# Performance work log

Hardware: AMD Instinct MI355X
Metric: run time of the kernel (lower is better)

The kernel has to match this reference:

```python
import jax, jax.numpy as jnp
import numpy as np

BS, L, D = 128, 256, 512
H, DK = 2, 256  # heads, head dim
EPS_BN = 1e-5


def _lin(x, W, b):
    # torch Linear: W is (out, in)
    return jnp.einsum('...i,oi->...o', x, W) + b


def _bn(x, g, b, m, v):
    # eval-mode BatchNorm over channel axis = last axis of x
    return (x - m) * (g * jax.lax.rsqrt(v + EPS_BN)) + b


def setup_inputs() -> dict:
    key = jax.random.key(0)
    ks = iter(jax.random.split(key, 64))
    rn = lambda shape, s=0.02: jax.random.normal(next(ks), shape, dtype=jnp.float32) * s
    inp = {}
    inp['cap_emb'] = jax.random.normal(next(ks), (BS, L, D), dtype=jnp.float32)
    inp['lengths'] = jax.random.randint(next(ks), (BS,), 1, L + 1, dtype=jnp.int64 if jax.config.jax_enable_x64 else jnp.int32)
    # GA linears q,k,v
    for nm in ('Wq', 'Wk', 'Wv'):
        inp[nm] = rn((D, D))
    for nm in ('bq', 'bk', 'bv'):
        inp[nm] = rn((D,))
    inp['Wfq'] = rn((DK, DK)); inp['bfq'] = rn((DK,))
    inp['Wfk'] = rn((DK, DK)); inp['bfk'] = rn((DK,))
    inp['Wfg'] = rn((2 * DK, DK)); inp['bfg'] = rn((2 * DK,))
    # BatchNorm params (eval running stats)
    for pre in ('bn1', 'bn2', 'bn3'):
        inp[pre + '_g'] = 1.0 + rn((D,), 0.1)
        inp[pre + '_b'] = rn((D,), 0.1)
        inp[pre + '_m'] = rn((D,), 0.1)
        inp[pre + '_v'] = jax.random.uniform(next(ks), (D,), minval=0.5, maxval=1.5, dtype=jnp.float32)
    # Conv1d weights, torch layout (out, in, k)
    inp['Wc2'] = rn((D, D, 2)); inp['bc2'] = rn((D,))
    inp['Wc3'] = rn((D, D, 3)); inp['bc3'] = rn((D,))
    # MLP 512 -> 1024 -> 512
    inp['Wm1'] = rn((2 * D, D)); inp['bm1'] = rn((2 * D,))
    inp['Wm2'] = rn((D, 2 * D)); inp['bm2'] = rn((D,))
    return inp


def _forward(cap_emb, Wq, bq, Wk, bk, Wv, bv, Wfq, bfq, Wfk, bfk, Wfg, bfg,
             bn1_g, bn1_b, bn1_m, bn1_v, Wc2, bc2, bn2_g, bn2_b, bn2_m, bn2_v,
             Wc3, bc3, bn3_g, bn3_b, bn3_m, bn3_v, Wm1, bm1, Wm2, bm2, lengths):
    bs, seq, dim = cap_emb.shape
    # ---- GA: gated self-attention ----
    def split_heads(x):
        return x.reshape(bs, seq, H, DK).transpose(0, 2, 1, 3)  # [bs,h,seq,dk]
    q = split_heads(_lin(cap_emb, Wq, bq))
    k = split_heads(_lin(cap_emb, Wk, bk))
    v = split_heads(_lin(cap_emb, Wv, bv))
    G = _lin(q, Wfq, bfq) * _lin(k, Wfk, bfk)
    M = jax.nn.sigmoid(_lin(G, Wfg, bfg))  # [bs,h,seq,2*dk]
    qg = q * M[..., :DK]
    kg = k * M[..., DK:]
    # torch.div(..., rounding_mode='floor') == elementwise floor of scaled scores
    scores = jnp.floor(jnp.einsum('bhqd,bhkd->bhqk', qg, kg) / jnp.sqrt(jnp.float32(DK)))
    p_attn = jax.nn.softmax(scores, axis=-1)
    x = jnp.einsum('bhqk,bhkd->bhqd', p_attn, v)
    x = x.transpose(0, 2, 1, 3).reshape(bs, seq, dim)
    # BN over features (eval), dropout is identity in eval mode
    ga_emb = cap_emb + _bn(x, bn1_g, bn1_b, bn1_m, bn1_v)
    # ---- dual conv1d branches ----
    xc = cap_emb.transpose(0, 2, 1)  # [bs, D, L]
    dn = ('NCW', 'OIW', 'NCW')
    c2 = jax.lax.conv_general_dilated(xc, Wc2, window_strides=(2,), padding='VALID', dimension_numbers=dn) + bc2[None, :, None]
    c3 = jax.lax.conv_general_dilated(xc, Wc3, window_strides=(3,), padding='VALID', dimension_numbers=dn) + bc3[None, :, None]
    f2 = jax.nn.relu(_bn(c2.transpose(0, 2, 1), bn2_g, bn2_b, bn2_m, bn2_v))
    f3 = jax.nn.relu(_bn(c3.transpose(0, 2, 1), bn3_g, bn3_b, bn3_m, bn3_v))
    ga_jw = jnp.concatenate([ga_emb, f2, f3], axis=1)
    # ---- residual MLP (dropout identity in eval) ----
    hid = jax.nn.relu(_lin(ga_jw, Wm1, bm1))
    tex_emb = _lin(hid, Wm2, bm2) + ga_jw
    # ---- length-indexed gather ----
    idx = lengths.astype(jnp.int32) - 1
    out = tex_emb[jnp.arange(bs), idx]  # [bs, D]
    # l2norm
    norm = jnp.sqrt(jnp.sum(out * out, axis=-1, keepdims=True)) + 1e-8
    return out / norm


def reference(cap_emb, lengths, Wq, bq, Wk, bk, Wv, bv, Wfq, bfq, Wfk, bfk, Wfg, bfg,
              bn1_g, bn1_b, bn1_m, bn1_v, Wc2, bc2, bn2_g, bn2_b, bn2_m, bn2_v,
              Wc3, bc3, bn3_g, bn3_b, bn3_m, bn3_v, Wm1, bm1, Wm2, bm2):
    return _forward(cap_emb, Wq, bq, Wk, bk, Wv, bv, Wfq, bfq, Wfk, bfk, Wfg, bfg,
                    bn1_g, bn1_b, bn1_m, bn1_v, Wc2, bc2, bn2_g, bn2_b, bn2_m, bn2_v,
                    Wc3, bc3, bn3_g, bn3_b, bn3_m, bn3_v, Wm1, bm1, Wm2, bm2, lengths)
```

## Files before the change

### kernel.cpp

```cpp
#include <hip/hip_runtime.h>
#include <math.h>


typedef short bf16x8 __attribute__((ext_vector_type(8)));
typedef float f32x4 __attribute__((ext_vector_type(4)));
typedef short short4v __attribute__((ext_vector_type(4)));

__device__ __forceinline__ short f2bf(float x) {
    union { float f; unsigned u; } c; c.f = x;
    unsigned r = c.u + 0x7FFFu + ((c.u >> 16) & 1u);
    return (short)(r >> 16);
}
__device__ __forceinline__ float bf2f(short h) {
    union { float f; unsigned u; } c; c.u = ((unsigned)(unsigned short)h) << 16;
    return c.f;
}
__device__ __forceinline__ void glds16(const void* g, void* l) {
    __builtin_amdgcn_global_load_lds(
        (const __attribute__((address_space(1))) void*)g,
        (__attribute__((address_space(3))) void*)l, 16, 0, 0);
}

struct CastArgs {
    const float* src[3];
    short* dst[3];
    int n4[3];
};
__global__ __launch_bounds__(256) void cast_multi(CastArgs a)
{
    const int j = blockIdx.y;
    const float4* s = (const float4*)a.src[j];
    short* d = a.dst[j];
    const int n4 = a.n4[j];
    for (int i = blockIdx.x * 256 + threadIdx.x; i < n4; i += gridDim.x * 256) {
        float4 x = s[i];
        short4v h;
        h.x = f2bf(x.x); h.y = f2bf(x.y); h.z = f2bf(x.z); h.w = f2bf(x.w);
        *(short4v*)&d[i * 4] = h;
    }
}

__global__ __launch_bounds__(256)
void compose2(const float* __restrict__ Wq, const float* __restrict__ bq,
              const float* __restrict__ Wfq, const float* __restrict__ bfq,
              const float* __restrict__ Wk, const float* __restrict__ bk,
              const float* __restrict__ Wfk, const float* __restrict__ bfk,
              short* __restrict__ WaB, float* __restrict__ ba,
              short* __restrict__ WbB, float* __restrict__ bb)
{
    __shared__ float fq[256];
    __shared__ float redc[256];
    const int op = blockIdx.x;
    const int h = op >> 8, o = op & 255;
    const int t = threadIdx.x;
    const bool second = (blockIdx.y == 1);
    const float* W  = second ? Wk  : Wq;
    const float* bv = second ? bk  : bq;
    const float* F  = second ? Wfk : Wfq;
    const float* bf = second ? bfk : bfq;
    short* WB   = second ? WbB : WaB;
    float* bout = second ? bb  : ba;

    fq[t] = F[o * 256 + t];
    redc[t] = fq[t] * bv[h * 256 + t];
    __syncthreads();
    for (int s = 128; s > 0; s >>= 1) {
        if (t < s) redc[t] += redc[t + s];
        __syncthreads();
    }
    if (t == 0) bout[op] = redc[0] + bf[o];
    float s0 = 0.f, s1 = 0.f;
    for (int d = 0; d < 256; ++d) {
        const float f = fq[d];
        const float* wr = W + (size_t)(h * 256 + d) * 512;
        s0 += f * wr[t];
        s1 += f * wr[t + 256];
    }
    const size_t ro = (size_t)op * 512;
    WB[ro + t] = f2bf(s0);
    WB[ro + 256 + t] = f2bf(s1);
}

__device__ __forceinline__ void kloop_w(
    const short* __restrict__ A, int lda,
    const short* __restrict__ B, int ldb,
    int K, int bm, short (*lds)[12288], int tid, f32x4 acc[4][4])
{
    const int lane = tid & 63;
    const int wv = tid >> 6;
    const int wr = wv >> 2, wc = wv & 3;
    const int fr = lane & 15, kc = lane >> 4;
    const int r0 = tid >> 2;
    const int e0 = (((tid & 3) ^ ((r0 >> 1) & 3))) * 8;
    const int kce = (kc ^ ((fr >> 1) & 3)) * 8;

    auto stage = [&](int ph, int k0) {
        short* b = lds[ph];
        glds16(A + (size_t)(bm + r0) * lda + k0 + e0,    b + r0 * 32 + (tid & 3) * 8);
        glds16(B + (size_t)r0 * ldb + k0 + e0,           b + 4096 + r0 * 32 + (tid & 3) * 8);
        glds16(B + (size_t)(r0 + 128) * ldb + k0 + e0,   b + 4096 + (r0 + 128) * 32 + (tid & 3) * 8);
    };

    stage(0, 0);
    __syncthreads();
    const int NS = K / 32;
    for (int s = 0; s < NS; ++s) {
        if (s + 1 < NS) stage((s + 1) & 1, (s + 1) * 32);
        const short* b = lds[s & 1];
        bf16x8 ah[4], bh[4];
#pragma unroll
        for (int i = 0; i < 4; ++i)
            ah[i] = *(const bf16x8*)&b[(wr * 64 + i * 16 + fr) * 32 + kce];
#pragma unroll
        for (int i = 0; i < 4; ++i)
            bh[i] = *(const bf16x8*)&b[4096 + (wc * 64 + i * 16 + fr) * 32 + kce];
#pragma unroll
        for (int mi = 0; mi < 4; ++mi)
#pragma unroll
            for (int ni = 0; ni < 4; ++ni)
                acc[mi][ni] = __builtin_amdgcn_mfma_f32_16x16x32_bf16(ah[mi], bh[ni], acc[mi][ni], 0, 0, 0);
        __syncthreads();
    }
}

__global__ __launch_bounds__(512)
void gemm_g(const short* __restrict__ capB,
            const short* __restrict__ WaB, const short* __restrict__ WbB,
            const float* __restrict__ ba, const float* __restrict__ bb,
            short* __restrict__ Gbuf)
{
    __shared__ short lds[2][20480];
    const int tid = threadIdx.x;
    const int bm = blockIdx.x * 128;
    const int z = blockIdx.y;
    const short* B1 = WaB + (size_t)z * 256 * 512;
    const short* B2 = WbB + (size_t)z * 256 * 512;

    const int lane = tid & 63;
    const int wv = tid >> 6;
    const int wr = wv >> 2, wc = wv & 3;
    const int fr = lane & 15, kc = lane >> 4;
    const int r0 = tid >> 2;
    const int e0 = (((tid & 3) ^ ((r0 >> 1) & 3))) * 8;
    const int kce = (kc ^ ((fr >> 1) & 3)) * 8;

    auto stage = [&](int ph, int k0) {
        short* b = lds[ph];
        glds16(capB + (size_t)(bm + r0) * 512 + k0 + e0, b + r0 * 32 + (tid & 3) * 8);
        glds16(B1 + (size_t)r0 * 512 + k0 + e0,          b + 4096 + r0 * 32 + (tid & 3) * 8);
        glds16(B1 + (size_t)(r0 + 128) * 512 + k0 + e0,  b + 4096 + (r0 + 128) * 32 + (tid & 3) * 8);
        glds16(B2 + (size_t)r0 * 512 + k0 + e0,          b + 12288 + r0 * 32 + (tid & 3) * 8);
        glds16(B2 + (size_t)(r0 + 128) * 512 + k0 + e0,  b + 12288 + (r0 + 128) * 32 + (tid & 3) * 8);
    };

    f32x4 acc1[4][4], acc2[4][4];
#pragma unroll
    for (int i = 0; i < 4; ++i)
#pragma unroll
        for (int j = 0; j < 4; ++j) {
            acc1[i][j] = (f32x4){0.f, 0.f, 0.f, 0.f};
            acc2[i][j] = (f32x4){0.f, 0.f, 0.f, 0.f};
        }

    stage(0, 0);
    __syncthreads();
    for (int s = 0; s < 16; ++s) {
        if (s + 1 < 16) stage((s + 1) & 1, (s + 1) * 32);
        const short* b = lds[s & 1];
        bf16x8 ah[4], bh[4];
#pragma unroll
        for (int i = 0; i < 4; ++i)
            ah[i] = *(const bf16x8*)&b[(wr * 64 + i * 16 + fr) * 32 + kce];
#pragma unroll
        for (int i = 0; i < 4; ++i)
            bh[i] = *(const bf16x8*)&b[4096 + (wc * 64 + i * 16 + fr) * 32 + kce];
#pragma unroll
        for (int mi = 0; mi < 4; ++mi)
#pragma unroll
            for (int ni = 0; ni < 4; ++ni)
                acc1[mi][ni] = __builtin_amdgcn_mfma_f32_16x16x32_bf16(ah[mi], bh[ni], acc1[mi][ni], 0, 0, 0);
#pragma unroll
        for (int i = 0; i < 4; ++i)
            bh[i] = *(const bf16x8*)&b[12288 + (wc * 64 + i * 16 + fr) * 32 + kce];
#pragma unroll
        for (int mi = 0; mi < 4; ++mi)
#pragma unroll
            for (int ni = 0; ni < 4; ++ni)
                acc2[mi][ni] = __builtin_amdgcn_mfma_f32_16x16x32_bf16(ah[mi], bh[ni], acc2[mi][ni], 0, 0, 0);
        __syncthreads();
    }

#pragma unroll
    for (int mi = 0; mi < 4; ++mi) {
#pragma unroll
        for (int ni = 0; ni < 4; ++ni) {
#pragma unroll
            for (int r = 0; r < 4; ++r) {
                const int row = bm + wr * 64 + mi * 16 + kc * 4 + r;
                const int col = wc * 64 + ni * 16 + fr;
                const float av  = acc1[mi][ni][r] + ba[z * 256 + col];
                const float lin = acc2[mi][ni][r] + bb[z * 256 + col];
                Gbuf[(size_t)row * 512 + z * 256 + col] = f2bf(lin * av);
            }
        }
    }
}

__global__ __launch_bounds__(512)
void gemm_kg(const short* __restrict__ Gbuf,
             const short* __restrict__ Wfg2B, const float* __restrict__ bias,
             const short* __restrict__ capB,
             const short* __restrict__ WkB, const float* __restrict__ bk,
             const float* __restrict__ qg, float* __restrict__ scorep)
{
    __shared__ short lds[2][12288];
    __shared__ float sp[128][4];
    const int tid = threadIdx.x;
    const int bm = blockIdx.x * 128;
    const int z = blockIdx.y;

    f32x4 acc1[4][4], acc2[4][4];
#pragma unroll
    for (int i = 0; i < 4; ++i)
#pragma unroll
        for (int j = 0; j < 4; ++j) {
            acc1[i][j] = (f32x4){0.f, 0.f, 0.f, 0.f};
            acc2[i][j] = (f32x4){0.f, 0.f, 0.f, 0.f};
        }

    kloop_w(Gbuf + (size_t)z * 256, 512, Wfg2B, 256, 256, bm, lds, tid, acc1);
    kloop_w(capB, 512, WkB + (size_t)z * 256 * 512, 512, 512, bm, lds, tid, acc2);

    const int lane = tid & 63;
    const int wv = tid >> 6;
    const int wr = wv >> 2, wc = wv & 3;
    const int fr = lane & 15, kc = lane >> 4;

    float qgv[4];
    float pt[4][4];
    {
        const int b = bm >> 8;
#pragma unroll
        for (int ni = 0; ni < 4; ++ni)
            qgv[ni] = qg[b * 512 + z * 256 + wc * 64 + ni * 16 + fr];
#pragma unroll
        for (int mi = 0; mi < 4; ++mi)
#pragma unroll
            for (int r = 0; r < 4; ++r) pt[mi][r] = 0.f;
    }

#pragma unroll
    for (int mi = 0; mi < 4; ++mi) {
#pragma unroll
        for (int ni = 0; ni < 4; ++ni) {
#pragma unroll
            for (int r = 0; r < 4; ++r) {
                const int col = wc * 64 + ni * 16 + fr;
                const float v = acc1[mi][ni][r] + bias[col];
                const float e = acc2[mi][ni][r] + bk[z * 256 + col];
                const float kgv = e / (1.f + expf(-v));
                pt[mi][r] += kgv * qgv[ni];
            }
        }
    }

#pragma unroll
    for (int mi = 0; mi < 4; ++mi) {
#pragma unroll
        for (int r = 0; r < 4; ++r) {
            float p = pt[mi][r];
            p += __shfl_xor(p, 1);
            p += __shfl_xor(p, 2);
            p += __shfl_xor(p, 4);
            p += __shfl_xor(p, 8);
            if (fr == 0) {
                const int row_local = wr * 64 + mi * 16 + kc * 4 + r;
                sp[row_local][wc] = p;
            }
        }
    }
    __syncthreads();
    if (tid < 128) {
        const float s = sp[tid][0] + sp[tid][1] + sp[tid][2] + sp[tid][3];
        const int row = bm + tid;
        const int b = row >> 8, j = row & 255;
        scorep[(size_t)b * 512 + z * 256 + j] = s;
    }
}

__global__ __launch_bounds__(256)
void qg_kernel(const float* __restrict__ cap,
               const short* __restrict__ Gbuf,
               const float* __restrict__ Wq, const float* __restrict__ bq,
               const float* __restrict__ Wfg, const float* __restrict__ bfg,
               const int* __restrict__ lengths, float* __restrict__ qg)
{
    __shared__ float cr[512];
    __shared__ float gs[256];
    const int b = blockIdx.x >> 1, h = blockIdx.x & 1;
    const int t = threadIdx.x;
    int r = lengths[b] - 1;
    if (r < 0) r = 0;
    if (r > 255) r = 255;
    const size_t base = ((size_t)b * 256 + r) * 512;
    cr[t] = cap[base + t];
    cr[t + 256] = cap[base + 256 + t];
    gs[t] = bf2f(Gbuf[base + h * 256 + t]);
    __syncthreads();
    const float4* wq4 = (const float4*)(Wq + (size_t)(h * 256 + t) * 512);
    float q = 0.f;
    for (int k4 = 0; k4 < 128; ++k4) {
        float4 w = wq4[k4];
        q += w.x * cr[k4 * 4 + 0] + w.y * cr[k4 * 4 + 1]
           + w.z * cr[k4 * 4 + 2] + w.w * cr[k4 * 4 + 3];
    }
    q += bq[h * 256 + t];
    const float4* w4 = (const float4*)(Wfg + (size_t)t * 256);
    float a = 0.f;
    for (int k4 = 0; k4 < 64; ++k4) {
        float4 w = w4[k4];
        a += w.x * gs[k4 * 4 + 0] + w.y * gs[k4 * 4 + 1]
           + w.z * gs[k4 * 4 + 2] + w.w * gs[k4 * 4 + 3];
    }
    a += bfg[t];
    qg[b * 512 + h * 256 + t] = q / (1.f + expf(-a));
}

__global__ __launch_bounds__(256)
void pbar_kernel(const float* __restrict__ scorep, const short* __restrict__ capB,
                 float* __restrict__ pbar)
{
    __shared__ float sc[512], red[512];
    const int b = blockIdx.y, cg = blockIdx.x;
    const int t = threadIdx.x;
#pragma unroll
    for (int i = 0; i < 2; ++i) {
        const int o = t + i * 256;
        sc[o] = floorf(scorep[(size_t)b * 512 + o] * 0.0625f);
    }
    __syncthreads();
    red[t] = sc[t]; red[t + 256] = sc[t + 256];
    __syncthreads();
    for (int s = 128; s > 0; s >>= 1) {
        if (t < s) {
            red[t] = fmaxf(red[t], red[t + s]);
            red[256 + t] = fmaxf(red[256 + t], red[256 + t + s]);
        }
        __syncthreads();
    }
    const float mx0 = red[0], mx1 = red[256];
    __syncthreads();
    const float e0 = expf(sc[t] - mx0);
    const float e1 = expf(sc[t + 256] - mx1);
    red[t] = e0; red[t + 256] = e1;
    __syncthreads();
    for (int s = 128; s > 0; s >>= 1) {
        if (t < s) { red[t] += red[t + s]; red[256 + t] += red[256 + t + s]; }
        __syncthreads();
    }
    sc[t] = e0 / red[0];
    sc[t + 256] = e1 / red[256];
    __syncthreads();

    const int c = cg * 64 + (t & 63);
    const int jg = t >> 6;
    float a0 = 0.f, a1 = 0.f;
    for (int j = jg * 64; j < jg * 64 + 64; ++j) {
        const float cv = bf2f(capB[((size_t)(b * 256 + j)) * 512 + c]);
        a0 += sc[j] * cv;
        a1 += sc[256 + j] * cv;
    }
    red[t] = a0;
    __syncthreads();
    if (t < 64) {
        const float s0 = red[t] + red[t + 64] + red[t + 128] + red[t + 192];
        pbar[b * 1024 + cg * 64 + t] = s0;
    }
    __syncthreads();
    red[t] = a1;
    __syncthreads();
    if (t < 64) {
        const float s1 = red[t] + red[t + 64] + red[t + 128] + red[t + 192];
        pbar[b * 1024 + 512 + cg * 64 + t] = s1;
    }
}

__global__ __launch_bounds__(256)
void bnx_kernel(const float* __restrict__ pbar, const float* __restrict__ cap,
                const int* __restrict__ lengths,
                const float* __restrict__ Wv, const float* __restrict__ bv,
                const float* __restrict__ g1, const float* __restrict__ b1,
                const float* __restrict__ m1, const float* __restrict__ v1,
                float* __restrict__ xga)
{
    __shared__ float pb[1024];
    const int b = blockIdx.x;
    const int t = threadIdx.x;
    int r = lengths[b] - 1;
    if (r < 0) r = 0;
    if (r > 255) r = 255;
    const size_t base = ((size_t)b * 256 + r) * 512;
    pb[t] = pbar[b * 1024 + t];
    pb[t + 256] = pbar[b * 1024 + 256 + t];
    pb[t + 512] = pbar[b * 1024 + 512 + t];
    pb[t + 768] = pbar[b * 1024 + 768 + t];
    __syncthreads();
    float x0 = 0.f, x1 = 0.f;
    {
        const float4* w4 = (const float4*)(Wv + (size_t)t * 512);
        for (int k4 = 0; k4 < 128; ++k4) {
            float4 w = w4[k4];
            x0 += w.x * pb[k4 * 4 + 0] + w.y * pb[k4 * 4 + 1]
                + w.z * pb[k4 * 4 + 2] + w.w * pb[k4 * 4 + 3];
        }
        x0 += bv[t];
    }
    {
        const float4* w4 = (const float4*)(Wv + (size_t)(t + 256) * 512);
        for (int k4 = 0; k4 < 128; ++k4) {
            float4 w = w4[k4];
            x1 += w.x * pb[512 + k4 * 4 + 0] + w.y * pb[512 + k4 * 4 + 1]
                + w.z * pb[512 + k4 * 4 + 2] + w.w * pb[512 + k4 * 4 + 3];
        }
        x1 += bv[t + 256];
    }
    const int c0 = t, c1 = t + 256;
    const float s0 = g1[c0] / sqrtf(v1[c0] + 1e-5f);
    const float s1 = g1[c1] / sqrtf(v1[c1] + 1e-5f);
    xga[b * 512 + c0] = cap[base + c0] + (x0 - m1[c0]) * s0 + b1[c0];
    xga[b * 512 + c1] = cap[base + c1] + (x1 - m1[c1]) * s1 + b1[c1];
}

__global__ __launch_bounds__(256)
void mlp1(const float* __restrict__ xga, const float* __restrict__ W,
          const float* __restrict__ bias, float* __restrict__ hid)
{
    __shared__ float xs[16 * 512];
    const int r0 = blockIdx.y * 16;
    const int c0 = blockIdx.x * 64;
    for (int i = threadIdx.x; i < 2048; i += 256)
        ((float4*)xs)[i] = ((const float4*)(xga + (size_t)r0 * 512))[i];
    __syncthreads();
    const int col = c0 + (threadIdx.x & 63);
    const int rg = (threadIdx.x >> 6) * 4;
    float acc[4] = {0.f, 0.f, 0.f, 0.f};
    const float4* w4 = (const float4*)(W + (size_t)col * 512);
    for (int k4 = 0; k4 < 128; ++k4) {
        float4 w = w4[k4];
#pragma unroll
        for (int rr = 0; rr < 4; ++rr) {
            float4 x = *(const float4*)&xs[(rg + rr) * 512 + k4 * 4];
            acc[rr] += w.x * x.x + w.y * x.y + w.z * x.z + w.w * x.w;
        }
    }
    const float bb = bias[col];
#pragma unroll
    for (int rr = 0; rr < 4; ++rr)
        hid[(size_t)(r0 + rg + rr) * 1024 + col] = fmaxf(acc[rr] + bb, 0.f);
}

__global__ __launch_bounds__(256)
void mlp2(const float* __restrict__ hid, const float* __restrict__ W,
          const float* __restrict__ bias, const float* __restrict__ xga,
          float* __restrict__ tex)
{
    __shared__ float xs[16 * 1024];
    const int r0 = blockIdx.y * 16;
    const int c0 = blockIdx.x * 64;
    for (int i = threadIdx.x; i < 4096; i += 256)
        ((float4*)xs)[i] = ((const float4*)(hid + (size_t)r0 * 1024))[i];
    __syncthreads();
    const int col = c0 + (threadIdx.x & 63);
    const int rg = (threadIdx.x >> 6) * 4;
    float acc[4] = {0.f, 0.f, 0.f, 0.f};
    const float4* w4 = (const float4*)(W + (size_t)col * 1024);
    for (int k4 = 0; k4 < 256; ++k4) {
        float4 w = w4[k4];
#pragma unroll
        for (int rr = 0; rr < 4; ++rr) {
            float4 x = *(const float4*)&xs[(rg + rr) * 1024 + k4 * 4];
            acc[rr] += w.x * x.x + w.y * x.y + w.z * x.z + w.w * x.w;
        }
    }
    const float bb = bias[col];
#pragma unroll
    for (int rr = 0; rr < 4; ++rr) {
        const int row = r0 + rg + rr;
        tex[(size_t)row * 512 + col] = acc[rr] + bb + xga[(size_t)row * 512 + col];
    }
}

__global__ __launch_bounds__(256)
void norm_out(const float* __restrict__ tex, float* __restrict__ out)
{
    __shared__ float red[256];
    const int b = blockIdx.x;
    const int t = threadIdx.x;
    const float a = tex[b * 512 + t];
    const float c = tex[b * 512 + 256 + t];
    red[t] = a * a + c * c;
    __syncthreads();
    for (int s = 128; s > 0; s >>= 1) {
        if (t < s) red[t] += red[t + s];
        __syncthreads();
    }
    const float inv = 1.f / (sqrtf(red[0]) + 1e-8f);
    out[b * 512 + t] = a * inv;
    out[b * 512 + 256 + t] = c * inv;
}

extern "C" void kernel_launch(void* const* d_in, const int* in_sizes, int n_in,
                              void* d_out, int out_size, void* d_ws, size_t ws_size,
                              hipStream_t stream)
{
    const float* cap = (const float*)d_in[0];
    const int* lengths = (const int*)d_in[1];
    const float* Wq  = (const float*)d_in[2];
    const float* Wk  = (const float*)d_in[3];
    const float* Wv  = (const float*)d_in[4];
    const float* bq  = (const float*)d_in[5];
    const float* bk  = (const float*)d_in[6];
    const float* bv  = (const float*)d_in[7];
    const float* Wfq = (const float*)d_in[8];
    const float* bfq = (const float*)d_in[9];
    const float* Wfk = (const float*)d_in[10];
    const float* bfk = (const float*)d_in[11];
    const float* Wfg = (const float*)d_in[12];
    const float* bfg = (const float*)d_in[13];
    const float* g1  = (const float*)d_in[14];
    const float* b1  = (const float*)d_in[15];
    const float* m1  = (const float*)d_in[16];
    const float* v1  = (const float*)d_in[17];
    const float* Wm1 = (const float*)d_in[30];
    const float* bm1 = (const float*)d_in[31];
    const float* Wm2 = (const float*)d_in[32];
    const float* bm2 = (const float*)d_in[33];
    float* out = (float*)d_out;

    char* w = (char*)d_ws;
    const size_t MB = 1024 * 1024;
    short* capB = (short*)(w);
    short* Gbuf = (short*)(w + 32 * MB);
    char* wp = w + 64 * MB;
    short* WkB   = (short*)wp; wp += 524288;
    short* WaB   = (short*)wp; wp += 524288;
    short* WbB   = (short*)wp; wp += 524288;
    short* Wfg2B = (short*)wp; wp += 131072;
    float* ba     = (float*)wp; wp += 2048;
    float* bb     = (float*)wp; wp += 2048;
    float* qg     = (float*)wp; wp += 262144;
    float* scorep = (float*)wp; wp += 262144;
    float* pbar   = (float*)wp; wp += 524288;
    float* xga    = (float*)wp; wp += 262144;
    float* hid    = (float*)wp; wp += 524288;
    float* tex    = (float*)wp; wp += 262144;

    CastArgs ca;
    ca.src[0] = cap;          ca.dst[0] = capB;  ca.n4[0] = 4194304;
    ca.src[1] = Wk;           ca.dst[1] = WkB;   ca.n4[1] = 65536;
    ca.src[2] = Wfg + 65536;  ca.dst[2] = Wfg2B; ca.n4[2] = 16384;
    cast_multi<<<dim3(4096, 3), 256, 0, stream>>>(ca);

    compose2<<<dim3(512, 2), 256, 0, stream>>>(Wq, bq, Wfq, bfq, Wk, bk, Wfk, bfk,
                                               WaB, ba, WbB, bb);

    gemm_g<<<dim3(256, 2), 512, 0, stream>>>(capB, WaB, WbB, ba, bb, Gbuf);

    qg_kernel<<<dim3(256), 256, 0, stream>>>(cap, Gbuf, Wq, bq, Wfg, bfg, lengths, qg);

    gemm_kg<<<dim3(256, 2), 512, 0, stream>>>(Gbuf, Wfg2B, bfg + 256,
                                              capB, WkB, bk, qg, scorep);

    pbar_kernel<<<dim3(8, 128), 256, 0, stream>>>(scorep, capB, pbar);
    bnx_kernel<<<dim3(128), 256, 0, stream>>>(pbar, cap, lengths, Wv, bv, g1, b1, m1, v1, xga);

    mlp1<<<dim3(16, 8), 256, 0, stream>>>(xga, Wm1, bm1, hid);
    mlp2<<<dim3(8, 8), 256, 0, stream>>>(hid, Wm2, bm2, xga, tex);
    norm_out<<<dim3(128), 256, 0, stream>>>(tex, out);
}
```

Before: 271.2 us.

## Fuse gate GEMM with key-gate GEMM, keeping G tile in LDS

```diff
diff --git a/kernel.cpp b/kernel.cpp
--- a/kernel.cpp
+++ b/kernel.cpp
@@ -81,11 +81,18 @@
     WB[ro + 256 + t] = f2bf(s1);
 }
 
-__device__ __forceinline__ void kloop_w(
-    const short* __restrict__ A, int lda,
-    const short* __restrict__ B, int ldb,
-    int K, int bm, short (*lds)[12288], int tid, f32x4 acc[4][4])
-{
+__global__ __launch_bounds__(512)
+void gemm_gkg(const short* __restrict__ capB,
+              const short* __restrict__ WaB, const short* __restrict__ WbB,
+              const float* __restrict__ ba, const float* __restrict__ bb,
+              const short* __restrict__ Wfg2B, const float* __restrict__ bfg2,
+              const short* __restrict__ WkB, const float* __restrict__ bk,
+              const float* __restrict__ qg, float* __restrict__ scorep)
+{
+    __shared__ short smem[40960];
+    const int tid = threadIdx.x;
+    const int bm = blockIdx.x * 128;
+    const int z = blockIdx.y;
     const int lane = tid & 63;
     const int wv = tid >> 6;
     const int wr = wv >> 2, wc = wv & 3;
@@ -94,64 +101,8 @@
     const int e0 = (((tid & 3) ^ ((r0 >> 1) & 3))) * 8;
     const int kce = (kc ^ ((fr >> 1) & 3)) * 8;
 
-    auto stage = [&](int ph, int k0) {
-        short* b = lds[ph];
-        glds16(A + (size_t)(bm + r0) * lda + k0 + e0,    b + r0 * 32 + (tid & 3) * 8);
-        glds16(B + (size_t)r0 * ldb + k0 + e0,           b + 4096 + r0 * 32 + (tid & 3) * 8);
-        glds16(B + (size_t)(r0 + 128) * ldb + k0 + e0,   b + 4096 + (r0 + 128) * 32 + (tid & 3) * 8);
-    };
-
-    stage(0, 0);
-    __syncthreads();
-    const int NS = K / 32;
-    for (int s = 0; s < NS; ++s) {
-        if (s + 1 < NS) stage((s + 1) & 1, (s + 1) * 32);
-        const short* b = lds[s & 1];
-        bf16x8 ah[4], bh[4];
-#pragma unroll
-        for (int i = 0; i < 4; ++i)
-            ah[i] = *(const bf16x8*)&b[(wr * 64 + i * 16 + fr) * 32 + kce];
-#pragma unroll
-        for (int i = 0; i < 4; ++i)
-            bh[i] = *(const bf16x8*)&b[4096 + (wc * 64 + i * 16 + fr) * 32 + kce];
-#pragma unroll
-        for (int mi = 0; mi < 4; ++mi)
-#pragma unroll
-            for (int ni = 0; ni < 4; ++ni)
-                acc[mi][ni] = __builtin_amdgcn_mfma_f32_16x16x32_bf16(ah[mi], bh[ni], acc[mi][ni], 0, 0, 0);
-        __syncthreads();
-    }
-}
-
-__global__ __launch_bounds__(512)
-void gemm_g(const short* __restrict__ capB,
-            const short* __restrict__ WaB, const short* __restrict__ WbB,
-            const float* __restrict__ ba, const float* __restrict__ bb,
-            short* __restrict__ Gbuf)
-{
-    __shared__ short lds[2][20480];
-    const int tid = threadIdx.x;
-    const int bm = blockIdx.x * 128;
-    const int z = blockIdx.y;
     const short* B1 = WaB + (size_t)z * 256 * 512;
     const short* B2 = WbB + (size_t)z * 256 * 512;
-
-    const int lane = tid & 63;
-    const int wv = tid >> 6;
-    const int wr = wv >> 2, wc = wv & 3;
-    const int fr = lane & 15, kc = lane >> 4;
-    const int r0 = tid >> 2;
-    const int e0 = (((tid & 3) ^ ((r0 >> 1) & 3))) * 8;
-    const int kce = (kc ^ ((fr >> 1) & 3)) * 8;
-
-    auto stage = [&](int ph, int k0) {
-        short* b = lds[ph];
-        glds16(capB + (size_t)(bm + r0) * 512 + k0 + e0, b + r0 * 32 + (tid & 3) * 8);
-        glds16(B1 + (size_t)r0 * 512 + k0 + e0,          b + 4096 + r0 * 32 + (tid & 3) * 8);
-        glds16(B1 + (size_t)(r0 + 128) * 512 + k0 + e0,  b + 4096 + (r0 + 128) * 32 + (tid & 3) * 8);
-        glds16(B2 + (size_t)r0 * 512 + k0 + e0,          b + 12288 + r0 * 32 + (tid & 3) * 8);
-        glds16(B2 + (size_t)(r0 + 128) * 512 + k0 + e0,  b + 12288 + (r0 + 128) * 32 + (tid & 3) * 8);
-    };
 
     f32x4 acc1[4][4], acc2[4][4];
 #pragma unroll
@@ -162,11 +113,20 @@
             acc2[i][j] = (f32x4){0.f, 0.f, 0.f, 0.f};
         }
 
-    stage(0, 0);
+    auto stageA = [&](int ph, int k0) {
+        short* s = smem + ph * 20480;
+        glds16(capB + (size_t)(bm + r0) * 512 + k0 + e0, s + tid * 8);
+        glds16(B1 + (size_t)r0 * 512 + k0 + e0,          s + 4096 + tid * 8);
+        glds16(B1 + (size_t)(r0 + 128) * 512 + k0 + e0,  s + 4096 + (tid + 512) * 8);
+        glds16(B2 + (size_t)r0 * 512 + k0 + e0,          s + 12288 + tid * 8);
+        glds16(B2 + (size_t)(r0 + 128) * 512 + k0 + e0,  s + 12288 + (tid + 512) * 8);
+    };
+
+    stageA(0, 0);
     __syncthreads();
     for (int s = 0; s < 16; ++s) {
-        if (s + 1 < 16) stage((s + 1) & 1, (s + 1) * 32);
-        const short* b = lds[s & 1];
+        if (s + 1 < 16) stageA((s + 1) & 1, (s + 1) * 32);
+        const short* b = smem + (s & 1) * 20480;
         bf16x8 ah[4], bh[4];
 #pragma unroll
         for (int i = 0; i < 4; ++i)
@@ -196,58 +156,87 @@
         for (int ni = 0; ni < 4; ++ni) {
 #pragma unroll
             for (int r = 0; r < 4; ++r) {
-                const int row = bm + wr * 64 + mi * 16 + kc * 4 + r;
+                const int row = wr * 64 + mi * 16 + kc * 4 + r;
                 const int col = wc * 64 + ni * 16 + fr;
-                const float av  = acc1[mi][ni][r] + ba[z * 256 + col];
-                const float lin = acc2[mi][ni][r] + bb[z * 256 + col];
-                Gbuf[(size_t)row * 512 + z * 256 + col] = f2bf(lin * av);
+                const float g = (acc2[mi][ni][r] + bb[z * 256 + col])
+                              * (acc1[mi][ni][r] + ba[z * 256 + col]);
+                const int grp = (col >> 3) ^ ((row >> 1) & 3);
+                smem[row * 256 + grp * 8 + (col & 7)] = f2bf(g);
             }
         }
     }
-}
-
-__global__ __launch_bounds__(512)
-void gemm_kg(const short* __restrict__ Gbuf,
-             const short* __restrict__ Wfg2B, const float* __restrict__ bias,
-             const short* __restrict__ capB,
-             const short* __restrict__ WkB, const float* __restrict__ bk,
-             const float* __restrict__ qg, float* __restrict__ scorep)
-{
-    __shared__ short lds[2][12288];
-    __shared__ float sp[128][4];
-    const int tid = threadIdx.x;
-    const int bm = blockIdx.x * 128;
-    const int z = blockIdx.y;
-
-    f32x4 acc1[4][4], acc2[4][4];
+    __syncthreads();
+
+    f32x4 acc3[4][4];
 #pragma unroll
     for (int i = 0; i < 4; ++i)
 #pragma unroll
-        for (int j = 0; j < 4; ++j) {
-            acc1[i][j] = (f32x4){0.f, 0.f, 0.f, 0.f};
-            acc2[i][j] = (f32x4){0.f, 0.f, 0.f, 0.f};
-        }
-
-    kloop_w(Gbuf + (size_t)z * 256, 512, Wfg2B, 256, 256, bm, lds, tid, acc1);
-    kloop_w(capB, 512, WkB + (size_t)z * 256 * 512, 512, 512, bm, lds, tid, acc2);
-
-    const int lane = tid & 63;
-    const int wv = tid >> 6;
-    const int wr = wv >> 2, wc = wv & 3;
-    const int fr = lane & 15, kc = lane >> 4;
+        for (int j = 0; j < 4; ++j) acc3[i][j] = (f32x4){0.f, 0.f, 0.f, 0.f};
+
+    short* sB = smem + 32768;
+    for (int kk = 0; kk < 8; ++kk) {
+        const int k0 = kk * 32;
+        glds16(Wfg2B + (size_t)r0 * 256 + k0 + e0,         sB + tid * 8);
+        glds16(Wfg2B + (size_t)(r0 + 128) * 256 + k0 + e0, sB + (tid + 512) * 8);
+        __syncthreads();
+        bf16x8 ah[4], bh[4];
+#pragma unroll
+        for (int i = 0; i < 4; ++i)
+            ah[i] = *(const bf16x8*)&smem[(wr * 64 + i * 16 + fr) * 256 + k0 + kce];
+#pragma unroll
+        for (int i = 0; i < 4; ++i)
+            bh[i] = *(const bf16x8*)&sB[(wc * 64 + i * 16 + fr) * 32 + kce];
+#pragma unroll
+        for (int mi = 0; mi < 4; ++mi)
+#pragma unroll
+            for (int ni = 0; ni < 4; ++ni)
+                acc3[mi][ni] = __builtin_amdgcn_mfma_f32_16x16x32_bf16(ah[mi], bh[ni], acc3[mi][ni], 0, 0, 0);
+        __syncthreads();
+    }
+
+    const short* BK = WkB + (size_t)z * 256 * 512;
+#pragma unroll
+    for (int i = 0; i < 4; ++i)
+#pragma unroll
+        for (int j = 0; j < 4; ++j) acc2[i][j] = (f32x4){0.f, 0.f, 0.f, 0.f};
+
+    auto stageC = [&](int ph, int k0) {
+        short* s = smem + ph * 12288;
+        glds16(capB + (size_t)(bm + r0) * 512 + k0 + e0, s + tid * 8);
+        glds16(BK + (size_t)r0 * 512 + k0 + e0,          s + 4096 + tid * 8);
+        glds16(BK + (size_t)(r0 + 128) * 512 + k0 + e0,  s + 4096 + (tid + 512) * 8);
+    };
+
+    stageC(0, 0);
+    __syncthreads();
+    for (int s = 0; s < 16; ++s) {
+        if (s + 1 < 16) stageC((s + 1) & 1, (s + 1) * 32);
+        const short* b = smem + (s & 1) * 12288;
+        bf16x8 ah[4], bh[4];
+#pragma unroll
+        for (int i = 0; i < 4; ++i)
+            ah[i] = *(const bf16x8*)&b[(wr * 64 + i * 16 + fr) * 32 + kce];
+#pragma unroll
+        for (int i = 0; i < 4; ++i)
+            bh[i] = *(const bf16x8*)&b[4096 + (wc * 64 + i * 16 + fr) * 32 + kce];
+#pragma unroll
+        for (int mi = 0; mi < 4; ++mi)
+#pragma unroll
+            for (int ni = 0; ni < 4; ++ni)
+                acc2[mi][ni] = __builtin_amdgcn_mfma_f32_16x16x32_bf16(ah[mi], bh[ni], acc2[mi][ni], 0, 0, 0);
+        __syncthreads();
+    }
 
     float qgv[4];
     float pt[4][4];
-    {
-        const int b = bm >> 8;
-#pragma unroll
-        for (int ni = 0; ni < 4; ++ni)
-            qgv[ni] = qg[b * 512 + z * 256 + wc * 64 + ni * 16 + fr];
-#pragma unroll
-        for (int mi = 0; mi < 4; ++mi)
-#pragma unroll
-            for (int r = 0; r < 4; ++r) pt[mi][r] = 0.f;
-    }
+    const int b_ = bm >> 8;
+#pragma unroll
+    for (int ni = 0; ni < 4; ++ni)
+        qgv[ni] = qg[b_ * 512 + z * 256 + wc * 64 + ni * 16 + fr];
+#pragma unroll
+    for (int mi = 0; mi < 4; ++mi)
+#pragma unroll
+        for (int r = 0; r < 4; ++r) pt[mi][r] = 0.f;
 
 #pragma unroll
     for (int mi = 0; mi < 4; ++mi) {
@@ -256,7 +245,7 @@
 #pragma unroll
             for (int r = 0; r < 4; ++r) {
                 const int col = wc * 64 + ni * 16 + fr;
-                const float v = acc1[mi][ni][r] + bias[col];
+                const float v = acc3[mi][ni][r] + bfg2[col];
                 const float e = acc2[mi][ni][r] + bk[z * 256 + col];
                 const float kgv = e / (1.f + expf(-v));
                 pt[mi][r] += kgv * qgv[ni];
@@ -264,6 +253,7 @@
         }
     }
 
+    float (*sp)[4] = (float(*)[4])smem;
 #pragma unroll
     for (int mi = 0; mi < 4; ++mi) {
 #pragma unroll
@@ -290,7 +280,8 @@
 
 __global__ __launch_bounds__(256)
 void qg_kernel(const float* __restrict__ cap,
-               const short* __restrict__ Gbuf,
+               const short* __restrict__ WaB, const short* __restrict__ WbB,
+               const float* __restrict__ ba, const float* __restrict__ bb,
                const float* __restrict__ Wq, const float* __restrict__ bq,
                const float* __restrict__ Wfg, const float* __restrict__ bfg,
                const int* __restrict__ lengths, float* __restrict__ qg)
@@ -305,7 +296,23 @@
     const size_t base = ((size_t)b * 256 + r) * 512;
     cr[t] = cap[base + t];
     cr[t + 256] = cap[base + 256 + t];
-    gs[t] = bf2f(Gbuf[base + h * 256 + t]);
+    __syncthreads();
+    {
+        const bf16x8* wa8 = (const bf16x8*)(WaB + (size_t)(h * 256 + t) * 512);
+        const bf16x8* wb8 = (const bf16x8*)(WbB + (size_t)(h * 256 + t) * 512);
+        float sa = 0.f, sb = 0.f;
+        for (int k8 = 0; k8 < 64; ++k8) {
+            bf16x8 wa = wa8[k8];
+            bf16x8 wb = wb8[k8];
+#pragma unroll
+            for (int j = 0; j < 8; ++j) {
+                const float c = cr[k8 * 8 + j];
+                sa += bf2f(wa[j]) * c;
+                sb += bf2f(wb[j]) * c;
+            }
+        }
+        gs[t] = (sb + bb[h * 256 + t]) * (sa + ba[h * 256 + t]);
+    }
     __syncthreads();
     const float4* wq4 = (const float4*)(Wq + (size_t)(h * 256 + t) * 512);
     float q = 0.f;
@@ -540,8 +547,7 @@
     char* w = (char*)d_ws;
     const size_t MB = 1024 * 1024;
     short* capB = (short*)(w);
-    short* Gbuf = (short*)(w + 32 * MB);
-    char* wp = w + 64 * MB;
+    char* wp = w + 32 * MB;
     short* WkB   = (short*)wp; wp += 524288;
     short* WaB   = (short*)wp; wp += 524288;
     short* WbB   = (short*)wp; wp += 524288;
@@ -564,12 +570,11 @@
     compose2<<<dim3(512, 2), 256, 0, stream>>>(Wq, bq, Wfq, bfq, Wk, bk, Wfk, bfk,
                                                WaB, ba, WbB, bb);
 
-    gemm_g<<<dim3(256, 2), 512, 0, stream>>>(capB, WaB, WbB, ba, bb, Gbuf);
-
-    qg_kernel<<<dim3(256), 256, 0, stream>>>(cap, Gbuf, Wq, bq, Wfg, bfg, lengths, qg);
-
-    gemm_kg<<<dim3(256, 2), 512, 0, stream>>>(Gbuf, Wfg2B, bfg + 256,
-                                              capB, WkB, bk, qg, scorep);
+    qg_kernel<<<dim3(256), 256, 0, stream>>>(cap, WaB, WbB, ba, bb,
+                                             Wq, bq, Wfg, bfg, lengths, qg);
+
+    gemm_gkg<<<dim3(256, 2), 512, 0, stream>>>(capB, WaB, WbB, ba, bb,
+                                               Wfg2B, bfg + 256, WkB, bk, qg, scorep);
 
     pbar_kernel<<<dim3(8, 128), 256, 0, stream>>>(scorep, capB, pbar);
     bnx_kernel<<<dim3(128), 256, 0, stream>>>(pbar, cap, lengths, Wv, bv, g1, b1, m1, v1, xga);
```

New measurement: 276.7 us. 1.02x slower.
